# Kernel optimization log

Measured on AMD Instinct MI355X. Metric: run time of the kernel, lower is better.

The kernel has to match this reference:

```python
import jax, jax.numpy as jnp
import numpy as np

D_MODEL, D_STATE, D_CONV, EXPAND, HEADDIM = 256, 16, 4, 2, 16
D_INNER = EXPAND * D_MODEL            # 512
NHEADS = D_INNER // HEADDIM           # 32
CONV_DIM = D_INNER + 2 * D_STATE      # 544 (ngroups=1)
D_IN_PROJ = 2 * D_INNER + 2 * D_STATE + NHEADS  # 1088
BATCH, SEQLEN = 8, 4096


def setup_inputs() -> dict:
    key = jax.random.key(0)
    ks = jax.random.split(key, 8)
    u = jax.random.normal(ks[0], (BATCH, SEQLEN, D_MODEL), jnp.float32)
    W_in = jax.random.normal(ks[1], (D_MODEL, D_IN_PROJ), jnp.float32) * 0.02
    conv_w = jax.random.normal(ks[2], (CONV_DIM, 1, D_CONV), jnp.float32) * 0.2
    conv_b = jnp.zeros((CONV_DIM,), jnp.float32)
    # dt_bias init: inverse-softplus of dt ~ Uniform in log-space [dt_min, dt_max]
    dt = jnp.exp(jax.random.uniform(ks[3], (NHEADS,), jnp.float32)
                 * (np.log(0.1) - np.log(0.001)) + np.log(0.001))
    dt = jnp.clip(dt, 1e-4, None)
    dt_bias = dt + jnp.log(-jnp.expm1(-dt))
    A_log = jnp.log(jax.random.uniform(ks[4], (NHEADS,), jnp.float32, 1.0, 16.0))
    D = jnp.ones((NHEADS,), jnp.float32)
    norm_w = jnp.ones((D_INNER,), jnp.float32)
    W_out = jax.random.normal(ks[5], (D_INNER, D_MODEL), jnp.float32) * 0.02
    return dict(u=u, W_in=W_in, conv_w=conv_w, conv_b=conv_b, dt_bias=dt_bias,
                A_log=A_log, D=D, norm_w=norm_w, W_out=W_out)


def _mamba2_forward(u, W_in, conv_w, conv_b, dt_bias, A_log, D, norm_w, W_out):
    batch, seqlen, _ = u.shape
    zxbcdt = u @ W_in                                   # (B, L, 2*d_inner + 2*N + H)
    z = zxbcdt[..., :D_INNER]                           # gate
    xBC = zxbcdt[..., D_INNER:2 * D_INNER + 2 * D_STATE]
    dt = jax.nn.softplus(zxbcdt[..., -NHEADS:] + dt_bias)  # (B, L, H)
    # causal depthwise conv1d over time + SiLU
    xc = jnp.transpose(xBC, (0, 2, 1))                  # (B, C, L)
    xc = jax.lax.conv_general_dilated(
        xc, conv_w, window_strides=(1,), padding=[(D_CONV - 1, 0)],
        feature_group_count=CONV_DIM, dimension_numbers=('NCH', 'OIH', 'NCH'))
    xBC = jax.nn.silu(jnp.transpose(xc, (0, 2, 1)) + conv_b)
    x = xBC[..., :D_INNER].reshape(batch, seqlen, NHEADS, HEADDIM)  # (B,L,H,P)
    Bm = xBC[..., D_INNER:D_INNER + D_STATE]            # (B, L, N), ngroups=1
    Cm = xBC[..., D_INNER + D_STATE:]                   # (B, L, N)
    A = -jnp.exp(A_log)                                 # (H,)
    dA = jnp.exp(dt * A)                                # (B, L, H) decay per step

    # selective scan: h_t = dA_t * h_{t-1} + dt_t * (B_t outer x_t); y_t = C_t . h_t
    def step(h, inp):
        da_t, dt_t, b_t, x_t, c_t = inp
        h = da_t[:, :, None, None] * h + jnp.einsum('bh,bn,bhp->bhpn', dt_t, b_t, x_t)
        y_t = jnp.einsum('bhpn,bn->bhp', h, c_t)
        return h, y_t

    h0 = jnp.zeros((batch, NHEADS, HEADDIM, D_STATE), u.dtype)
    xs = (jnp.moveaxis(dA, 1, 0), jnp.moveaxis(dt, 1, 0),
          jnp.moveaxis(Bm, 1, 0), jnp.moveaxis(x, 1, 0), jnp.moveaxis(Cm, 1, 0))
    _, ys = jax.lax.scan(step, h0, xs)                  # ys: (L, B, H, P)
    y = jnp.moveaxis(ys, 0, 1) + D[None, None, :, None] * x
    y = y.reshape(batch, seqlen, D_INNER)
    # gated RMSNorm (norm_before_gate=False): normalize(y * silu(z)) * weight
    t = y * jax.nn.silu(z)
    t = t * jax.lax.rsqrt(jnp.mean(t * t, axis=-1, keepdims=True) + 1e-5) * norm_w
    return t @ W_out


def reference(u, W_in, conv_w, conv_b, dt_bias, A_log, D, norm_w, W_out):
    return _mamba2_forward(u, W_in, conv_w, conv_b, dt_bias, A_log, D, norm_w, W_out)
```

## Files before the change

kernel.cpp:

```cpp
#include <hip/hip_runtime.h>
#include <hip/hip_bf16.h>
#include <math.h>

#define BATCH   8
#define SEQLEN  4096
#define DMODEL  256
#define DSTATE  16
#define NHEADS  32
#define HEADDIM 16
#define DINNER  512
#define CONVDIM 544
#define DINPROJ 1088
#define NROWS   (BATCH*SEQLEN)
#define CHUNK   64
#define NCH     (SEQLEN/CHUNK)

typedef __attribute__((ext_vector_type(8))) short short8;
typedef __attribute__((ext_vector_type(8))) unsigned short ushort8;
typedef __attribute__((ext_vector_type(4))) float f32x4;

__device__ __forceinline__ float bfu2f(unsigned short u){
  union { float f; unsigned int i; } x; x.i = ((unsigned int)u) << 16; return x.f;
}
__device__ __forceinline__ unsigned short f2bfu(float f){
  union { float f; unsigned int u; } v; v.f = f;
  v.u += 0x7fffu + ((v.u >> 16) & 1u);
  return (unsigned short)(v.u >> 16);
}

__global__ __launch_bounds__(256) void k_cast_u(const float* __restrict__ u, unsigned short* __restrict__ ub){
  int i = blockIdx.x*256 + threadIdx.x;
  float4 v = reinterpret_cast<const float4*>(u)[i];
  ushort4 o; o.x=f2bfu(v.x); o.y=f2bfu(v.y); o.z=f2bfu(v.z); o.w=f2bfu(v.w);
  reinterpret_cast<ushort4*>(ub)[i] = o;
}

__global__ __launch_bounds__(256) void k_transpose_cast(const float* __restrict__ W, unsigned short* __restrict__ WT, int K, int N){
  int idx = blockIdx.x*256 + threadIdx.x;
  if (idx >= N*K) return;
  int n = idx / K, k = idx - n*K;
  WT[idx] = f2bfu(W[(size_t)k*N + n]);
}

template<int EPI>
__global__ __launch_bounds__(256) void k_gemm(
    const unsigned short* __restrict__ A,
    const unsigned short* __restrict__ BT,
    int M, int N, int K,
    unsigned short* __restrict__ oz,
    unsigned short* __restrict__ oxbc,
    float* __restrict__ odtraw,
    float* __restrict__ of32)
{
  __shared__ uint4 lds[768];
  const int tid = threadIdx.x;
  const int lane = tid & 63;
  const int wid = tid >> 6;
  const int wr = wid >> 1, wc = wid & 1;
  const int bm0 = blockIdx.x * 128;
  const int bn0 = blockIdx.y * 64;
  const int fr = lane & 15, kq = lane >> 4;
  f32x4 acc[4][2] = {};
  const int nK = K >> 5;
  for (int kt = 0; kt < nK; ++kt){
    const int k0 = kt << 5;
    #pragma unroll
    for (int i = 0; i < 2; ++i){
      int c = tid + i*256;
      int row = c >> 2, slot = c & 3;
      uint4 v = *reinterpret_cast<const uint4*>(A + (size_t)(bm0+row)*K + k0 + slot*8);
      lds[row*4 + (slot ^ (row & 3))] = v;
    }
    {
      int row = tid >> 2, slot = tid & 3;
      uint4 v = *reinterpret_cast<const uint4*>(BT + (size_t)(bn0+row)*K + k0 + slot*8);
      lds[512 + row*4 + (slot ^ (row & 3))] = v;
    }
    __syncthreads();
    short8 bfrag[2];
    #pragma unroll
    for (int nf = 0; nf < 2; ++nf){
      int rb = wc*32 + nf*16 + fr;
      bfrag[nf] = *reinterpret_cast<const short8*>(&lds[512 + rb*4 + (kq ^ (rb & 3))]);
    }
    #pragma unroll
    for (int mf = 0; mf < 4; ++mf){
      int ra = wr*64 + mf*16 + fr;
      short8 afrag = *reinterpret_cast<const short8*>(&lds[ra*4 + (kq ^ (ra & 3))]);
      #pragma unroll
      for (int nf = 0; nf < 2; ++nf)
        acc[mf][nf] = __builtin_amdgcn_mfma_f32_16x16x32_bf16(afrag, bfrag[nf], acc[mf][nf], 0, 0, 0);
    }
    __syncthreads();
  }
  #pragma unroll
  for (int mf = 0; mf < 4; ++mf){
    #pragma unroll
    for (int nf = 0; nf < 2; ++nf){
      #pragma unroll
      for (int r = 0; r < 4; ++r){
        int m = bm0 + wr*64 + mf*16 + kq*4 + r;
        int n = bn0 + wc*32 + nf*16 + fr;
        float v = acc[mf][nf][r];
        if (EPI == 1){
          if (n < DINNER)                 oz[(size_t)m*DINNER + n] = f2bfu(v);
          else if (n < DINNER + CONVDIM)  oxbc[(size_t)m*CONVDIM + (n - DINNER)] = f2bfu(v);
          else                            odtraw[(size_t)m*NHEADS + (n - DINNER - CONVDIM)] = v;
        } else {
          of32[(size_t)m*N + n] = v;
        }
      }
    }
  }
}

__global__ __launch_bounds__(256) void k_convbc(const unsigned short* __restrict__ xbc,
                                                const float* __restrict__ cw,
                                                const float* __restrict__ cb,
                                                float* __restrict__ bco){
  const int tid = threadIdx.x;
  const int j = tid & 31;
  const int rt = tid >> 5;
  const int r0 = blockIdx.x*64 + rt*8;
  const int ch = 512 + j;
  const int tloc = r0 & (SEQLEN-1);
  float wv0 = cw[ch*4+0], wv1 = cw[ch*4+1], wv2 = cw[ch*4+2], wv3 = cw[ch*4+3];
  const float bias = cb[ch];
  float xr[11];
  #pragma unroll
  for (int k = 0; k < 11; ++k){
    int r = r0 - 3 + k;
    xr[k] = (tloc - 3 + k < 0) ? 0.f : bfu2f(xbc[(size_t)r*CONVDIM + ch]);
  }
  #pragma unroll
  for (int i = 0; i < 8; ++i){
    float acc = fmaf(wv0, xr[i], fmaf(wv1, xr[i+1], fmaf(wv2, xr[i+2], fmaf(wv3, xr[i+3], bias))));
    bco[(size_t)(r0+i)*32 + j] = acc / (1.f + __expf(-acc));
  }
}

__global__ __launch_bounds__(256) void k_dtda(const float* __restrict__ dtraw,
                                              const float* __restrict__ dt_bias,
                                              const float* __restrict__ A_log,
                                              float* __restrict__ dt_o,
                                              float* __restrict__ dA_o){
  int i = blockIdx.x*256 + threadIdx.x;
  int h = i & (NHEADS-1);
  float x = dtraw[i] + dt_bias[h];
  float dt = (x > 20.f) ? x : log1pf(expf(x));
  dt_o[i] = dt;
  dA_o[i] = expf(-expf(A_log[h]) * dt);
}

__global__ __launch_bounds__(256,4) void k_scan1(
    const unsigned short* __restrict__ xbc, const float* __restrict__ bc,
    const float* __restrict__ dta, const float* __restrict__ daa,
    const float* __restrict__ cwv, const float* __restrict__ cbv,
    const float* __restrict__ Dv,
    float* __restrict__ yl, float* __restrict__ st, float* __restrict__ Pp)
{
  __shared__ float sBC[65*32];
  __shared__ float sdt[65*16];
  __shared__ float sda[65*16];
  const int tid = threadIdx.x;
  const int bid = blockIdx.x;
  const int qh = bid & 1;
  const int c  = (bid >> 1) & (NCH-1);
  const int b  = bid >> 7;
  const int w  = tid >> 6;
  const int l  = tid & 63;
  const int q  = qh*4 + w;
  const int hh = l >> 4, p = l & 15;
  const int h  = q*4 + hh;
  const size_t row0 = (size_t)b*SEQLEN + (size_t)c*CHUNK;
  const int xoff = q*64 + l;
  {
    const float* src = bc + row0*32;
    #pragma unroll
    for (int i = 0; i < 2; ++i){
      int idx = tid + i*256;
      *reinterpret_cast<float4*>(&sBC[idx*4]) = *reinterpret_cast<const float4*>(src + (size_t)idx*4);
    }
  }
  {
    int t = tid >> 2, g = (tid & 3)*4;
    *reinterpret_cast<float4*>(&sdt[t*16+g]) =
      *reinterpret_cast<const float4*>(dta + (row0+t)*NHEADS + qh*16 + g);
    *reinterpret_cast<float4*>(&sda[t*16+g]) =
      *reinterpret_cast<const float4*>(daa + (row0+t)*NHEADS + qh*16 + g);
  }
  const float cw0 = cwv[xoff*4+0], cw1 = cwv[xoff*4+1], cw2 = cwv[xoff*4+2], cw3 = cwv[xoff*4+3];
  const float cb0 = cbv[xoff];
  const float Dh = Dv[h];
  const int dIdx = w*4 + hh;
  float wA, wB, wC;
  if (c == 0){ wA = wB = wC = 0.f; }
  else {
    wA = bfu2f(xbc[(row0-3)*CONVDIM + xoff]);
    wB = bfu2f(xbc[(row0-2)*CONVDIM + xoff]);
    wC = bfu2f(xbc[(row0-1)*CONVDIM + xoff]);
  }
  float xq0 = bfu2f(xbc[(row0+0)*CONVDIM + xoff]);
  float xq1 = bfu2f(xbc[(row0+1)*CONVDIM + xoff]);
  float xq2 = bfu2f(xbc[(row0+2)*CONVDIM + xoff]);
  float xq3 = bfu2f(xbc[(row0+3)*CONVDIM + xoff]);
  __syncthreads();
  float BA[32], BB[32];
  #pragma unroll
  for (int k = 0; k < 8; ++k)
    *reinterpret_cast<float4*>(&BA[4*k]) = *reinterpret_cast<const float4*>(&sBC[4*k]);
  float dtA = sdt[dIdx], daA = sda[dIdx];
  float dtB, daB;
  float hs[16];
  #pragma unroll
  for (int n = 0; n < 16; ++n) hs[n] = 0.f;
  float cum = 1.f;

#define S1STEP(CUR, NXT, DTC, DAC, DTN, DAN, XQ, T) {                          \
    const int t_ = (T);                                                        \
    _Pragma("unroll")                                                          \
    for (int k = 0; k < 8; ++k)                                                \
      *reinterpret_cast<float4*>(&NXT[4*k]) =                                  \
        *reinterpret_cast<const float4*>(&sBC[(t_+1)*32 + 4*k]);               \
    DTN = sdt[(t_+1)*16 + dIdx]; DAN = sda[(t_+1)*16 + dIdx];                  \
    float xnew = bfu2f(xbc[(row0 + t_ + 4)*CONVDIM + xoff]);                   \
    float xc = fmaf(cw0, wA, fmaf(cw1, wB, fmaf(cw2, wC, fmaf(cw3, XQ, cb0))));\
    wA = wB; wB = wC; wC = XQ; XQ = xnew;                                      \
    float xs = xc / (1.f + __expf(-xc));                                       \
    float dx = DTC * xs;                                                       \
    float y_ = 0.f;                                                            \
    _Pragma("unroll")                                                          \
    for (int n = 0; n < 16; ++n) hs[n] = fmaf(DAC, hs[n], dx*CUR[n]);          \
    _Pragma("unroll")                                                          \
    for (int n = 0; n < 16; ++n) y_ = fmaf(hs[n], CUR[16+n], y_);              \
    cum *= DAC;                                                                \
    yl[(row0 + t_)*DINNER + xoff] = y_ + Dh*xs;                                \
  }

  for (int T = 0; T < CHUNK; T += 4){
    S1STEP(BA, BB, dtA, daA, dtB, daB, xq0, T+0);
    S1STEP(BB, BA, dtB, daB, dtA, daA, xq1, T+1);
    S1STEP(BA, BB, dtA, daA, dtB, daB, xq2, T+2);
    S1STEP(BB, BA, dtB, daB, dtA, daA, xq3, T+3);
  }
#undef S1STEP
  float* sp = st + (((size_t)(b*NHEADS + h)*NCH + c)*16 + p)*16;
  #pragma unroll
  for (int k = 0; k < 4; ++k)
    *reinterpret_cast<float4*>(sp + 4*k) = make_float4(hs[4*k], hs[4*k+1], hs[4*k+2], hs[4*k+3]);
  if (p == 0) Pp[((size_t)b*NHEADS + h)*NCH + c] = cum;
}

__global__ __launch_bounds__(64) void k_scan2(float* __restrict__ st, const float* __restrict__ Pp){
  const int bh = blockIdx.x;
  const int l = threadIdx.x;
  float* sb = st + (size_t)bh*NCH*256 + l*4;
  const float* pb = Pp + (size_t)bh*NCH;
  float4 carry = make_float4(0.f,0.f,0.f,0.f);
  float4 Hb[4]; float Pb[4];
  #pragma unroll
  for (int i = 0; i < 4; ++i){
    Hb[i] = *reinterpret_cast<const float4*>(sb + (size_t)i*256);
    Pb[i] = pb[i];
  }
  for (int c0 = 0; c0 < NCH; c0 += 4){
    #pragma unroll
    for (int i = 0; i < 4; ++i){
      const int cc = c0 + i;
      float4 Hc = Hb[i]; float Pc = Pb[i];
      if (cc + 4 < NCH){
        Hb[i] = *reinterpret_cast<const float4*>(sb + (size_t)(cc+4)*256);
        Pb[i] = pb[cc+4];
      }
      *reinterpret_cast<float4*>(sb + (size_t)cc*256) = carry;
      carry.x = fmaf(Pc, carry.x, Hc.x);
      carry.y = fmaf(Pc, carry.y, Hc.y);
      carry.z = fmaf(Pc, carry.z, Hc.z);
      carry.w = fmaf(Pc, carry.w, Hc.w);
    }
  }
}

__global__ __launch_bounds__(256,4) void k_scan3(
    const float* __restrict__ yl, const float* __restrict__ bc,
    const float* __restrict__ daa, const float* __restrict__ st,
    unsigned short* __restrict__ ybf)
{
  __shared__ float sC[65*16];
  __shared__ float sda[65*16];
  const int tid = threadIdx.x;
  const int bid = blockIdx.x;
  const int qh = bid & 1;
  const int c  = (bid >> 1) & (NCH-1);
  const int b  = bid >> 7;
  const int w  = tid >> 6;
  const int l  = tid & 63;
  const int q  = qh*4 + w;
  const int hh = l >> 4, p = l & 15;
  const int h  = q*4 + hh;
  const size_t row0 = (size_t)b*SEQLEN + (size_t)c*CHUNK;
  const int xoff = q*64 + l;
  {
    int t = tid >> 2, g = (tid & 3)*4;
    *reinterpret_cast<float4*>(&sC[t*16+g]) =
      *reinterpret_cast<const float4*>(bc + (row0+t)*32 + 16 + g);
    *reinterpret_cast<float4*>(&sda[t*16+g]) =
      *reinterpret_cast<const float4*>(daa + (row0+t)*NHEADS + qh*16 + g);
  }
  float hi[16];
  {
    const float* sp = st + (((size_t)(b*NHEADS + h)*NCH + c)*16 + p)*16;
    #pragma unroll
    for (int k = 0; k < 4; ++k){
      float4 v = *reinterpret_cast<const float4*>(sp + 4*k);
      hi[4*k] = v.x; hi[4*k+1] = v.y; hi[4*k+2] = v.z; hi[4*k+3] = v.w;
    }
  }
  float yq0 = yl[(row0+0)*DINNER + xoff];
  float yq1 = yl[(row0+1)*DINNER + xoff];
  float yq2 = yl[(row0+2)*DINNER + xoff];
  float yq3 = yl[(row0+3)*DINNER + xoff];
  __syncthreads();
  const int dIdx = w*4 + hh;
  float CA[16], CB[16];
  #pragma unroll
  for (int k = 0; k < 4; ++k)
    *reinterpret_cast<float4*>(&CA[4*k]) = *reinterpret_cast<const float4*>(&sC[4*k]);
  float daA = sda[dIdx], daB;
  float cum = 1.f;

#define S3STEP(CUR, NXT, DAC, DAN, YQ, T) {                                    \
    const int t_ = (T);                                                        \
    _Pragma("unroll")                                                          \
    for (int k = 0; k < 4; ++k)                                                \
      *reinterpret_cast<float4*>(&NXT[4*k]) =                                  \
        *reinterpret_cast<const float4*>(&sC[(t_+1)*16 + 4*k]);                \
    DAN = sda[(t_+1)*16 + dIdx];                                               \
    float ynew = yl[(row0 + t_ + 4)*DINNER + xoff];                            \
    cum *= DAC;                                                                \
    float corr = 0.f;                                                          \
    _Pragma("unroll")                                                          \
    for (int n = 0; n < 16; ++n) corr = fmaf(hi[n], CUR[n], corr);             \
    ybf[(row0 + t_)*DINNER + xoff] = f2bfu(YQ + cum*corr);                     \
    YQ = ynew;                                                                 \
  }

  for (int T = 0; T < CHUNK; T += 4){
    S3STEP(CA, CB, daA, daB, yq0, T+0);
    S3STEP(CB, CA, daB, daA, yq1, T+1);
    S3STEP(CA, CB, daA, daB, yq2, T+2);
    S3STEP(CB, CA, daB, daA, yq3, T+3);
  }
#undef S3STEP
}

__global__ __launch_bounds__(256) void k_gate(const unsigned short* __restrict__ ybf,
                                              unsigned short* __restrict__ zbf,
                                              const float* __restrict__ nw){
  int row = blockIdx.x*4 + (threadIdx.x >> 6);
  int l = threadIdx.x & 63;
  size_t base = (size_t)row*DINNER + l*8;
  ushort8 yv = *reinterpret_cast<const ushort8*>(ybf + base);
  ushort8 zv = *reinterpret_cast<const ushort8*>(zbf + base);
  float tv[8]; float ss = 0.f;
  #pragma unroll
  for (int j = 0; j < 8; ++j){
    float yf = bfu2f(yv[j]);
    float zf = bfu2f(zv[j]);
    float s = zf / (1.f + __expf(-zf));
    float t = yf * s; tv[j] = t; ss += t*t;
  }
  #pragma unroll
  for (int m = 1; m <= 32; m <<= 1) ss += __shfl_xor(ss, m, 64);
  float scale = rsqrtf(ss * (1.f/DINNER) + 1e-5f);
  ushort8 o;
  #pragma unroll
  for (int j = 0; j < 8; ++j) o[j] = f2bfu(tv[j] * scale * nw[l*8+j]);
  *reinterpret_cast<ushort8*>(zbf + base) = o;
}

extern "C" void kernel_launch(void* const* d_in, const int* in_sizes, int n_in,
                              void* d_out, int out_size, void* d_ws, size_t ws_size,
                              hipStream_t stream)
{
  const float* u       = (const float*)d_in[0];
  const float* W_in    = (const float*)d_in[1];
  const float* conv_w  = (const float*)d_in[2];
  const float* conv_b  = (const float*)d_in[3];
  const float* dt_bias = (const float*)d_in[4];
  const float* A_log   = (const float*)d_in[5];
  const float* Dvec    = (const float*)d_in[6];
  const float* norm_w  = (const float*)d_in[7];
  const float* W_out   = (const float*)d_in[8];
  float* out = (float*)d_out;
  char* ws = (char*)d_ws;

  unsigned short* ubf   = (unsigned short*)(ws + 0);
  float* chst           = (float*)(ws + 0);
  unsigned short* wintT = (unsigned short*)(ws + 16777216);
  unsigned short* woutT = (unsigned short*)(ws + 17334272);
  unsigned short* zbf   = (unsigned short*)(ws + 17596416);
  unsigned short* xbcbf = (unsigned short*)(ws + 51150848);
  float* dtraw          = (float*)(ws + 86802432);
  float* Pp             = dtraw;
  float* ylocal         = (float*)(ws + 90996736);
  float* convoBC        = (float*)(ws + 158105600);
  float* dtq            = (float*)(ws + 162299904);
  float* daq            = (float*)(ws + 166494208);
  unsigned short* ybf   = xbcbf;

  k_cast_u<<<NROWS*DMODEL/1024, 256, 0, stream>>>(u, ubf);
  k_transpose_cast<<<(DINPROJ*DMODEL+255)/256, 256, 0, stream>>>(W_in, wintT, DMODEL, DINPROJ);
  k_transpose_cast<<<(DINNER*DMODEL+255)/256, 256, 0, stream>>>(W_out, woutT, DINNER, DMODEL);

  dim3 g1(NROWS/128, DINPROJ/64);
  k_gemm<1><<<g1, 256, 0, stream>>>(ubf, wintT, NROWS, DINPROJ, DMODEL, zbf, xbcbf, dtraw, nullptr);

  k_convbc<<<NROWS/64, 256, 0, stream>>>(xbcbf, conv_w, conv_b, convoBC);
  k_dtda<<<NROWS*NHEADS/256, 256, 0, stream>>>(dtraw, dt_bias, A_log, dtq, daq);

  k_scan1<<<BATCH*2*NCH, 256, 0, stream>>>(xbcbf, convoBC, dtq, daq, conv_w, conv_b, Dvec,
                                           ylocal, chst, Pp);
  k_scan2<<<BATCH*NHEADS, 64, 0, stream>>>(chst, Pp);
  k_scan3<<<BATCH*2*NCH, 256, 0, stream>>>(ylocal, convoBC, daq, chst, ybf);

  k_gate<<<NROWS/4, 256, 0, stream>>>(ybf, zbf, norm_w);

  dim3 g2(NROWS/128, DMODEL/64);
  k_gemm<2><<<g2, 256, 0, stream>>>(zbf, woutT, NROWS, DMODEL, DINNER, nullptr, nullptr, nullptr, out);
}
```

Measured before the change: 180.3 us.

## Double-buffer GEMM with direct global-to-LDS loads and wider N tiles

Rewrites the bf16 MFMA GEMM to use global_load_lds directly into a double-buffered LDS tile, prefetching the next K slice while computing the current one. This removes the register staging and one barrier per iteration. The N tile is templated: the input projection runs as 128-wide tiles over the first 1024 columns plus a 64-wide tail launch, and the output projection uses 128-wide tiles. The cost is larger LDS use per block and an extra kernel launch, which may reduce occupancy.

Result: no change. 177.0 us (-1.8%).

```diff
diff --git a/kernel.cpp b/kernel.cpp
--- a/kernel.cpp
+++ b/kernel.cpp
@@ -19,6 +19,9 @@
 typedef __attribute__((ext_vector_type(8))) unsigned short ushort8;
 typedef __attribute__((ext_vector_type(4))) float f32x4;
 
+#define LDSP(x) ((__attribute__((address_space(3))) void*)(x))
+#define GLBP(x) ((const __attribute__((address_space(1))) void*)(x))
+
 __device__ __forceinline__ float bfu2f(unsigned short u){
   union { float f; unsigned int i; } x; x.i = ((unsigned int)u) << 16; return x.f;
 }
@@ -42,72 +45,90 @@
   WT[idx] = f2bfu(W[(size_t)k*N + n]);
 }
 
-template<int EPI>
+template<int EPI, int BN>
 __global__ __launch_bounds__(256) void k_gemm(
     const unsigned short* __restrict__ A,
     const unsigned short* __restrict__ BT,
-    int M, int N, int K,
+    int K, int nbase,
     unsigned short* __restrict__ oz,
     unsigned short* __restrict__ oxbc,
     float* __restrict__ odtraw,
-    float* __restrict__ of32)
+    float* __restrict__ of32, int Nout)
 {
-  __shared__ uint4 lds[768];
+  constexpr int ABYTES = 128*64;
+  constexpr int BBYTES = BN*64;
+  constexpr int BUFB   = ABYTES + BBYTES;
+  constexpr int NF     = BN/32;
+  constexpr int BCALLS = BBYTES/4096;
+  __shared__ __align__(16) unsigned char lds[2*BUFB];
   const int tid = threadIdx.x;
-  const int lane = tid & 63;
-  const int wid = tid >> 6;
-  const int wr = wid >> 1, wc = wid & 1;
+  const int l   = tid & 63;
+  const int w   = tid >> 6;
+  const int wr  = w >> 1, wc = w & 1;
   const int bm0 = blockIdx.x * 128;
-  const int bn0 = blockIdx.y * 64;
-  const int fr = lane & 15, kq = lane >> 4;
-  f32x4 acc[4][2] = {};
+  const int bn0 = nbase + blockIdx.y * BN;
+  const int fr  = l & 15, kq = l >> 4;
+  f32x4 acc[4][NF] = {};
+
+  auto STAGE = [&](int buf, int kt){
+    const int k0 = kt << 5;
+    unsigned char* lb = (unsigned char*)lds + buf*BUFB;
+    #pragma unroll
+    for (int i = 0; i < 2; ++i){
+      int row = w*32 + i*16 + (l>>2);
+      int sl  = (l&3) ^ ((row>>1)&3);
+      const unsigned short* gp = A + (size_t)(bm0+row)*K + k0 + sl*8;
+      __builtin_amdgcn_global_load_lds(GLBP(gp), LDSP(lb + w*2048 + i*1024), 16, 0, 0);
+    }
+    #pragma unroll
+    for (int i = 0; i < BCALLS; ++i){
+      int row = w*(BCALLS*16) + i*16 + (l>>2);
+      int sl  = (l&3) ^ ((row>>1)&3);
+      const unsigned short* gp = BT + (size_t)(bn0+row)*K + k0 + sl*8;
+      __builtin_amdgcn_global_load_lds(GLBP(gp), LDSP(lb + ABYTES + w*(BCALLS*1024) + i*1024), 16, 0, 0);
+    }
+  };
+
   const int nK = K >> 5;
+  STAGE(0, 0);
+  __syncthreads();
+  int cur = 0;
   for (int kt = 0; kt < nK; ++kt){
-    const int k0 = kt << 5;
-    #pragma unroll
-    for (int i = 0; i < 2; ++i){
-      int c = tid + i*256;
-      int row = c >> 2, slot = c & 3;
-      uint4 v = *reinterpret_cast<const uint4*>(A + (size_t)(bm0+row)*K + k0 + slot*8);
-      lds[row*4 + (slot ^ (row & 3))] = v;
-    }
-    {
-      int row = tid >> 2, slot = tid & 3;
-      uint4 v = *reinterpret_cast<const uint4*>(BT + (size_t)(bn0+row)*K + k0 + slot*8);
-      lds[512 + row*4 + (slot ^ (row & 3))] = v;
-    }
-    __syncthreads();
-    short8 bfrag[2];
-    #pragma unroll
-    for (int nf = 0; nf < 2; ++nf){
-      int rb = wc*32 + nf*16 + fr;
-      bfrag[nf] = *reinterpret_cast<const short8*>(&lds[512 + rb*4 + (kq ^ (rb & 3))]);
+    if (kt + 1 < nK) STAGE(cur^1, kt+1);
+    const unsigned char* ab = (const unsigned char*)lds + cur*BUFB;
+    const unsigned char* bb = ab + ABYTES;
+    short8 bf[NF];
+    #pragma unroll
+    for (int nf = 0; nf < NF; ++nf){
+      int rb = wc*(BN/2) + nf*16 + fr;
+      bf[nf] = *reinterpret_cast<const short8*>(bb + rb*64 + ((kq ^ ((rb>>1)&3))*16));
     }
     #pragma unroll
     for (int mf = 0; mf < 4; ++mf){
       int ra = wr*64 + mf*16 + fr;
-      short8 afrag = *reinterpret_cast<const short8*>(&lds[ra*4 + (kq ^ (ra & 3))]);
+      short8 af = *reinterpret_cast<const short8*>(ab + ra*64 + ((kq ^ ((ra>>1)&3))*16));
       #pragma unroll
-      for (int nf = 0; nf < 2; ++nf)
-        acc[mf][nf] = __builtin_amdgcn_mfma_f32_16x16x32_bf16(afrag, bfrag[nf], acc[mf][nf], 0, 0, 0);
+      for (int nf = 0; nf < NF; ++nf)
+        acc[mf][nf] = __builtin_amdgcn_mfma_f32_16x16x32_bf16(af, bf[nf], acc[mf][nf], 0, 0, 0);
     }
     __syncthreads();
+    cur ^= 1;
   }
   #pragma unroll
   for (int mf = 0; mf < 4; ++mf){
     #pragma unroll
-    for (int nf = 0; nf < 2; ++nf){
+    for (int nf = 0; nf < NF; ++nf){
       #pragma unroll
       for (int r = 0; r < 4; ++r){
         int m = bm0 + wr*64 + mf*16 + kq*4 + r;
-        int n = bn0 + wc*32 + nf*16 + fr;
+        int n = bn0 + wc*(BN/2) + nf*16 + fr;
         float v = acc[mf][nf][r];
         if (EPI == 1){
           if (n < DINNER)                 oz[(size_t)m*DINNER + n] = f2bfu(v);
           else if (n < DINNER + CONVDIM)  oxbc[(size_t)m*CONVDIM + (n - DINNER)] = f2bfu(v);
           else                            odtraw[(size_t)m*NHEADS + (n - DINNER - CONVDIM)] = v;
         } else {
-          of32[(size_t)m*N + n] = v;
+          of32[(size_t)m*Nout + n] = v;
         }
       }
     }
@@ -413,8 +434,10 @@
   k_transpose_cast<<<(DINPROJ*DMODEL+255)/256, 256, 0, stream>>>(W_in, wintT, DMODEL, DINPROJ);
   k_transpose_cast<<<(DINNER*DMODEL+255)/256, 256, 0, stream>>>(W_out, woutT, DINNER, DMODEL);
 
-  dim3 g1(NROWS/128, DINPROJ/64);
-  k_gemm<1><<<g1, 256, 0, stream>>>(ubf, wintT, NROWS, DINPROJ, DMODEL, zbf, xbcbf, dtraw, nullptr);
+  dim3 g1a(NROWS/128, 1024/128);
+  k_gemm<1,128><<<g1a, 256, 0, stream>>>(ubf, wintT, DMODEL, 0, zbf, xbcbf, dtraw, nullptr, 0);
+  dim3 g1b(NROWS/128, 1);
+  k_gemm<1,64><<<g1b, 256, 0, stream>>>(ubf, wintT, DMODEL, 1024, zbf, xbcbf, dtraw, nullptr, 0);
 
   k_convbc<<<NROWS/64, 256, 0, stream>>>(xbcbf, conv_w, conv_b, convoBC);
   k_dtda<<<NROWS*NHEADS/256, 256, 0, stream>>>(dtraw, dt_bias, A_log, dtq, daq);
@@ -426,6 +449,6 @@
 
   k_gate<<<NROWS/4, 256, 0, stream>>>(ybf, zbf, norm_w);
 
-  dim3 g2(NROWS/128, DMODEL/64);
-  k_gemm<2><<<g2, 256, 0, stream>>>(zbf, woutT, NROWS, DMODEL, DINNER, nullptr, nullptr, nullptr, out);
-}
+  dim3 g2(NROWS/128, DMODEL/128);
+  k_gemm<2,128><<<g2, 256, 0, stream>>>(zbf, woutT, DINNER, 0, nullptr, nullptr, nullptr, out, DMODEL);
+}
```

## Widen GEMM tiles to 128 columns with XCD-aware block swizzle and templated K

Applied to the files above, without the earlier changes.

Templates the bf16 MFMA GEMM on wave-column count, K and a grid-swizzle parameter. Blocks now cover 128x128 tiles with 512 threads, and the flattened block index is remapped so consecutive blocks on the same XCD share A rows. The in-projection is split into a 1024-column wide launch plus a 64-column tail launch, and the out-projection uses the wider tile. The aim is to cut redundant A-tile reloads and improve L2 locality, at the cost of an extra launch and a larger per-block LDS footprint that may lower occupancy.

Result: no change. 177.0 us (-1.8%).

```diff
diff --git a/kernel.cpp b/kernel.cpp
--- a/kernel.cpp
+++ b/kernel.cpp
@@ -42,31 +42,42 @@
   WT[idx] = f2bfu(W[(size_t)k*N + n]);
 }
 
-template<int EPI>
-__global__ __launch_bounds__(256) void k_gemm(
+template<int EPI, int WC, int K, int NYL2>
+__global__ __launch_bounds__(WC*128) void k_gemm(
     const unsigned short* __restrict__ A,
     const unsigned short* __restrict__ BT,
-    int M, int N, int K,
+    int nbase,
     unsigned short* __restrict__ oz,
     unsigned short* __restrict__ oxbc,
     float* __restrict__ odtraw,
-    float* __restrict__ of32)
+    float* __restrict__ of32, int Nout)
 {
-  __shared__ uint4 lds[768];
+  constexpr int BN = WC*32;
+  constexpr int NAI = 4/WC;
+  __shared__ uint4 lds[512 + BN*4];
   const int tid = threadIdx.x;
-  const int lane = tid & 63;
-  const int wid = tid >> 6;
-  const int wr = wid >> 1, wc = wid & 1;
-  const int bm0 = blockIdx.x * 128;
-  const int bn0 = blockIdx.y * 64;
-  const int fr = lane & 15, kq = lane >> 4;
+  const int l   = tid & 63;
+  const int w   = tid >> 6;
+  const int wr  = w & 1, wc = w >> 1;
+  int bx, by;
+  if (NYL2 == 0){ bx = blockIdx.x; by = 0; }
+  else {
+    int flat = blockIdx.x;
+    int xcd = flat & 7;
+    int grp = flat >> 3;
+    by = grp & ((1 << NYL2) - 1);
+    bx = (grp >> NYL2)*8 + xcd;
+  }
+  const int bm0 = bx * 128;
+  const int bn0 = nbase + by * BN;
+  const int fr  = l & 15, kq = l >> 4;
   f32x4 acc[4][2] = {};
   const int nK = K >> 5;
   for (int kt = 0; kt < nK; ++kt){
     const int k0 = kt << 5;
     #pragma unroll
-    for (int i = 0; i < 2; ++i){
-      int c = tid + i*256;
+    for (int i = 0; i < NAI; ++i){
+      int c = tid + i*(WC*128);
       int row = c >> 2, slot = c & 3;
       uint4 v = *reinterpret_cast<const uint4*>(A + (size_t)(bm0+row)*K + k0 + slot*8);
       lds[row*4 + (slot ^ (row & 3))] = v;
@@ -107,7 +118,7 @@
           else if (n < DINNER + CONVDIM)  oxbc[(size_t)m*CONVDIM + (n - DINNER)] = f2bfu(v);
           else                            odtraw[(size_t)m*NHEADS + (n - DINNER - CONVDIM)] = v;
         } else {
-          of32[(size_t)m*N + n] = v;
+          of32[(size_t)m*Nout + n] = v;
         }
       }
     }
@@ -413,8 +424,8 @@
   k_transpose_cast<<<(DINPROJ*DMODEL+255)/256, 256, 0, stream>>>(W_in, wintT, DMODEL, DINPROJ);
   k_transpose_cast<<<(DINNER*DMODEL+255)/256, 256, 0, stream>>>(W_out, woutT, DINNER, DMODEL);
 
-  dim3 g1(NROWS/128, DINPROJ/64);
-  k_gemm<1><<<g1, 256, 0, stream>>>(ubf, wintT, NROWS, DINPROJ, DMODEL, zbf, xbcbf, dtraw, nullptr);
+  k_gemm<1,4,DMODEL,3><<<(NROWS/128)*8, 512, 0, stream>>>(ubf, wintT, 0, zbf, xbcbf, dtraw, nullptr, 0);
+  k_gemm<1,2,DMODEL,0><<<NROWS/128, 256, 0, stream>>>(ubf, wintT, 1024, zbf, xbcbf, dtraw, nullptr, 0);
 
   k_convbc<<<NROWS/64, 256, 0, stream>>>(xbcbf, conv_w, conv_b, convoBC);
   k_dtda<<<NROWS*NHEADS/256, 256, 0, stream>>>(dtraw, dt_bias, A_log, dtq, daq);
@@ -426,6 +437,5 @@
 
   k_gate<<<NROWS/4, 256, 0, stream>>>(ybf, zbf, norm_w);
 
-  dim3 g2(NROWS/128, DMODEL/64);
-  k_gemm<2><<<g2, 256, 0, stream>>>(zbf, woutT, NROWS, DMODEL, DINNER, nullptr, nullptr, nullptr, out);
-}
+  k_gemm<2,4,DINNER,1><<<(NROWS/128)*2, 512, 0, stream>>>(zbf, woutT, 0, nullptr, nullptr, nullptr, out, DMODEL);
+}
```
